# Performance work log

Measured on AMD Instinct MI355X. Metric: run time of the kernel, lower is better.

The kernel has to match this reference:

```python
import jax, jax.numpy as jnp
import numpy as np

T, N, D, G, H = 52, 1000, 2, 150, 50


def _mlp_scalar(x, W1, b1, W2, b2):
    # Elementwise scalar-input MLP: x [T,N,D] -> [T,N,D]
    h = jnp.tanh(x[..., None] * W1[0] + b1)          # [T,N,D,H]
    return jnp.einsum('tndh,h->tnd', h, W2[:, 0]) + b2[0]


def setup_inputs() -> dict:
    key = jax.random.key(0)
    ks = jax.random.split(key, 18)
    f = lambda k, s: jax.random.normal(k, s, dtype=jnp.float32)
    return {
        'TX': f(ks[0], (T, N, D)),
        't': jnp.arange(T, dtype=jnp.float32) * 0.01,
        'gaussn_0': f(ks[1], (G, T - 2, N)),
        'gaussn_1': f(ks[2], (G, T - 2, N, D)),
        'gaussn_2': f(ks[3], (G, T - 2, N, D)),
        'gaussnp1_1': f(ks[4], (G, T - 2, N, D)),
        'gaussnp1_2': f(ks[5], (G, T - 2, N, D)),
        'gaussnp2_0': f(ks[6], (G, T - 2, N)),
        'gaussnp2_1': f(ks[7], (G, T - 2, N, D)),
        'gaussnp2_2': f(ks[8], (G, T - 2, N, D)),
        'Wd1': f(ks[9], (1, H)) * 0.5,
        'bd1': jnp.zeros((H,), jnp.float32),
        'Wd2': f(ks[10], (H, 1)) * (1.0 / np.sqrt(H)),
        'bd2': jnp.zeros((1,), jnp.float32),
        'Ws1': f(ks[11], (1, H)) * 0.5,
        'bs1': jnp.zeros((H,), jnp.float32),
        'Ws2': f(ks[12], (H, 1)) * (1.0 / np.sqrt(H)),
        'bs2': jnp.zeros((1,), jnp.float32),
    }


def reference(TX, t, gaussn_0, gaussn_1, gaussn_2, gaussnp1_1, gaussnp1_2,
              gaussnp2_0, gaussnp2_1, gaussnp2_2,
              Wd1, bd1, Wd2, bd2, Ws1, bs1, Ws2, bs2):
    n = TX.shape[1]
    drift = _mlp_scalar(TX, Wd1, bd1, Wd2, bd2)            # [T,N,D]
    Dh = 0.5 * _mlp_scalar(TX, Ws1, bs1, Ws2, bs2)          # [T,N,D]

    def proj(g1, g2, a):
        # sum over d then mean over n == einsum over (n,d) / n -> [G, T-2]
        return (jnp.einsum('gtnd,tnd->gt', g1, a[0])
                + jnp.einsum('gtnd,tnd->gt', g2, a[1])) / n

    An = proj(gaussn_1, gaussn_2, (drift[:-2], Dh[:-2]))
    Anp1 = proj(gaussnp1_1, gaussnp1_2, (drift[1:-1], Dh[1:-1]))
    Anp2 = proj(gaussnp2_1, gaussnp2_2, (drift[2:], Dh[2:]))

    dt = (jnp.max(t) - jnp.min(t)) / (TX.shape[0] - 1)
    Aq = (An + 4.0 * Anp1 + Anp2) / 3.0 * dt                # LMM_3
    bq = jnp.mean(gaussnp2_0, axis=2) - jnp.mean(gaussn_0, axis=2)
    return (Aq - bq).reshape(-1)                            # [G*(T-2)]
```

## Files before the change

### kernel.cpp

```cpp
#include <hip/hip_runtime.h>
#include <hip/hip_bf16.h>

#define T_   52
#define N_   1000
#define D_   2
#define G_   150
#define H_   50
#define TM2  (T_ - 2)
#define ND   (N_ * D_)
#define TND  (T_ * N_ * D_)

typedef unsigned short ushort8_t __attribute__((ext_vector_type(8)));
typedef float          float8_t  __attribute__((ext_vector_type(8)));

__device__ __forceinline__ float bf2f(unsigned short u) {
    return __uint_as_float(((unsigned)u) << 16);
}
__device__ __forceinline__ unsigned short f2bf(float f) {
    unsigned u = __float_as_uint(f);
    u += 0x7fffu + ((u >> 16) & 1u);
    return (unsigned short)(u >> 16);
}

template<bool F32>
__device__ __forceinline__ float ld1(const void* p, int i) {
    if constexpr (F32) return ((const float*)p)[i];
    else               return bf2f(((const unsigned short*)p)[i]);
}

template<bool F32>
__device__ __forceinline__ float8_t ld8(const void* p, int i) {
    if constexpr (F32) {
        return *(const float8_t*)((const float*)p + i);
    } else {
        ushort8_t v = *(const ushort8_t*)((const unsigned short*)p + i);
        float8_t r;
#pragma unroll
        for (int j = 0; j < 8; ++j) r[j] = bf2f(v[j]);
        return r;
    }
}

template<bool F32>
__device__ __forceinline__ void mlp_body(
    const void* __restrict__ TX,
    const void* __restrict__ Wd1, const void* __restrict__ bd1,
    const void* __restrict__ Wd2, const void* __restrict__ bd2,
    const void* __restrict__ Ws1, const void* __restrict__ bs1,
    const void* __restrict__ Ws2, const void* __restrict__ bs2,
    float* __restrict__ drift, float* __restrict__ Dh)
{
    __shared__ float sW[6][H_];
    const int tid = threadIdx.x;
    if (tid < H_) {
        sW[0][tid] = ld1<F32>(Wd1, tid);
        sW[1][tid] = ld1<F32>(bd1, tid);
        sW[2][tid] = ld1<F32>(Wd2, tid);
        sW[3][tid] = ld1<F32>(Ws1, tid);
        sW[4][tid] = ld1<F32>(bs1, tid);
        sW[5][tid] = ld1<F32>(Ws2, tid);
    }
    __syncthreads();
    const int i = blockIdx.x * 256 + tid;
    if (i >= TND) return;
    const float x = ld1<F32>(TX, i);
    float accd = 0.f, accs = 0.f;
#pragma unroll 10
    for (int h = 0; h < H_; ++h) {
        accd += tanhf(fmaf(x, sW[0][h], sW[1][h])) * sW[2][h];
        accs += tanhf(fmaf(x, sW[3][h], sW[4][h])) * sW[5][h];
    }
    drift[i] = accd + ld1<F32>(bd2, 0);
    Dh[i]    = 0.5f * (accs + ld1<F32>(bs2, 0));
}

__global__ __launch_bounds__(256) void mlp_kernel(
    const void* TX,
    const void* Wd1, const void* bd1, const void* Wd2, const void* bd2,
    const void* Ws1, const void* bs1, const void* Ws2, const void* bs2,
    const void* t, float* drift, float* Dh)
{
    if (((const unsigned*)t)[0] == 0u)
        mlp_body<true>(TX, Wd1, bd1, Wd2, bd2, Ws1, bs1, Ws2, bs2, drift, Dh);
    else
        mlp_body<false>(TX, Wd1, bd1, Wd2, bd2, Ws1, bs1, Ws2, bs2, drift, Dh);
}

template<bool F32>
__device__ __forceinline__ void proj_body(
    const void* __restrict__ gn0,  const void* __restrict__ gn1,
    const void* __restrict__ gn2,  const void* __restrict__ gp11,
    const void* __restrict__ gp12, const void* __restrict__ gp20,
    const void* __restrict__ gp21, const void* __restrict__ gp22,
    const float* __restrict__ drift, const float* __restrict__ Dh,
    const void* __restrict__ t, void* __restrict__ out)
{
    const int gid = blockIdx.x;
    const int tp  = gid % TM2;
    const int tid = threadIdx.x;

    float acc = 0.f, bacc = 0.f;

    if (tid < ND / 8) {
        const int base = gid * ND + tid * 8;
        const float8_t a1 = ld8<F32>(gn1,  base);
        const float8_t a2 = ld8<F32>(gn2,  base);
        const float8_t b1 = ld8<F32>(gp11, base);
        const float8_t b2 = ld8<F32>(gp12, base);
        const float8_t c1 = ld8<F32>(gp21, base);
        const float8_t c2 = ld8<F32>(gp22, base);
        const int cb = tp * ND + tid * 8;
        const float8_t d0 = *(const float8_t*)(drift + cb);
        const float8_t h0 = *(const float8_t*)(Dh    + cb);
        const float8_t d1 = *(const float8_t*)(drift + cb + ND);
        const float8_t h1 = *(const float8_t*)(Dh    + cb + ND);
        const float8_t d2 = *(const float8_t*)(drift + cb + 2 * ND);
        const float8_t h2 = *(const float8_t*)(Dh    + cb + 2 * ND);
#pragma unroll
        for (int j = 0; j < 8; ++j) {
            acc += a1[j] * d0[j] + a2[j] * h0[j]
                 + 4.f * (b1[j] * d1[j] + b2[j] * h1[j])
                 + c1[j] * d2[j] + c2[j] * h2[j];
        }
    }
    if (tid < N_ / 8) {
        const int b0 = gid * N_ + tid * 8;
        const float8_t z0 = ld8<F32>(gn0,  b0);
        const float8_t z2 = ld8<F32>(gp20, b0);
#pragma unroll
        for (int j = 0; j < 8; ++j) bacc += z2[j] - z0[j];
    }

#pragma unroll
    for (int off = 32; off > 0; off >>= 1) {
        acc  += __shfl_down(acc, off);
        bacc += __shfl_down(bacc, off);
    }
    __shared__ float sA[4], sB[4];
    const int wave = tid >> 6, lane = tid & 63;
    if (lane == 0) { sA[wave] = acc; sB[wave] = bacc; }
    __syncthreads();
    if (tid == 0) {
        const float A = sA[0] + sA[1] + sA[2] + sA[3];
        const float B = sB[0] + sB[1] + sB[2] + sB[3];
        const float dt = (ld1<F32>(t, T_ - 1) - ld1<F32>(t, 0)) * (1.0f / (T_ - 1));
        const float val = A * (dt / (3.0f * (float)N_)) - B * (1.0f / (float)N_);
        if constexpr (F32) ((float*)out)[gid] = val;
        else               ((unsigned short*)out)[gid] = f2bf(val);
    }
}

__global__ __launch_bounds__(256) void proj_kernel(
    const void* gn0,  const void* gn1,  const void* gn2,
    const void* gp11, const void* gp12, const void* gp20,
    const void* gp21, const void* gp22,
    const float* drift, const float* Dh,
    const void* t, void* out)
{
    if (((const unsigned*)t)[0] == 0u)
        proj_body<true>(gn0, gn1, gn2, gp11, gp12, gp20, gp21, gp22,
                        drift, Dh, t, out);
    else
        proj_body<false>(gn0, gn1, gn2, gp11, gp12, gp20, gp21, gp22,
                         drift, Dh, t, out);
}

extern "C" void kernel_launch(void* const* d_in, const int* in_sizes, int n_in,
                              void* d_out, int out_size, void* d_ws, size_t ws_size,
                              hipStream_t stream) {
    const void* TX   = d_in[0];
    const void* t    = d_in[1];
    const void* gn0  = d_in[2];
    const void* gn1  = d_in[3];
    const void* gn2  = d_in[4];
    const void* gp11 = d_in[5];
    const void* gp12 = d_in[6];
    const void* gp20 = d_in[7];
    const void* gp21 = d_in[8];
    const void* gp22 = d_in[9];
    const void* Wd1  = d_in[10];
    const void* bd1  = d_in[11];
    const void* Wd2  = d_in[12];
    const void* bd2  = d_in[13];
    const void* Ws1  = d_in[14];
    const void* bs1  = d_in[15];
    const void* Ws2  = d_in[16];
    const void* bs2  = d_in[17];

    float* drift = (float*)d_ws;
    float* Dh    = drift + TND;

    mlp_kernel<<<(TND + 255) / 256, 256, 0, stream>>>(
        TX, Wd1, bd1, Wd2, bd2, Ws1, bs1, Ws2, bs2, t, drift, Dh);

    proj_kernel<<<G_ * TM2, 256, 0, stream>>>(
        gn0, gn1, gn2, gp11, gp12, gp20, gp21, gp22, drift, Dh, t,
        (void*)d_out);
}
```

Measured before the change: 401.0 us.

## Process CHUNK g-values per block to reuse drift/Dh loads in projection

Each projection block now handles six g indices at one time step instead of a single (g,t) pair. The drift/Dh vectors are loaded once per block and reused across the chunk, and the factor of 4 is folded into them. This cuts redundant workspace reads and the block count from 7500 to 1250. The cost is more registers per thread and fewer blocks, which may reduce latency hiding on a kernel bound by streaming the gaussian arrays.

Result: no change. 403.0 us (+0.5%).

```diff
diff --git a/kernel.cpp b/kernel.cpp
--- a/kernel.cpp
+++ b/kernel.cpp
@@ -9,6 +9,7 @@
 #define TM2  (T_ - 2)
 #define ND   (N_ * D_)
 #define TND  (T_ * N_ * D_)
+#define CHUNK 6
 
 typedef unsigned short ushort8_t __attribute__((ext_vector_type(8)));
 typedef float          float8_t  __attribute__((ext_vector_type(8)));
@@ -95,58 +96,81 @@
     const float* __restrict__ drift, const float* __restrict__ Dh,
     const void* __restrict__ t, void* __restrict__ out)
 {
-    const int gid = blockIdx.x;
-    const int tp  = gid % TM2;
+    const int tp  = blockIdx.x;
+    const int g0  = blockIdx.y * CHUNK;
     const int tid = threadIdx.x;
 
-    float acc = 0.f, bacc = 0.f;
+    float acc[CHUNK], bacc[CHUNK];
+#pragma unroll
+    for (int k = 0; k < CHUNK; ++k) { acc[k] = 0.f; bacc[k] = 0.f; }
 
     if (tid < ND / 8) {
-        const int base = gid * ND + tid * 8;
-        const float8_t a1 = ld8<F32>(gn1,  base);
-        const float8_t a2 = ld8<F32>(gn2,  base);
-        const float8_t b1 = ld8<F32>(gp11, base);
-        const float8_t b2 = ld8<F32>(gp12, base);
-        const float8_t c1 = ld8<F32>(gp21, base);
-        const float8_t c2 = ld8<F32>(gp22, base);
         const int cb = tp * ND + tid * 8;
         const float8_t d0 = *(const float8_t*)(drift + cb);
         const float8_t h0 = *(const float8_t*)(Dh    + cb);
-        const float8_t d1 = *(const float8_t*)(drift + cb + ND);
-        const float8_t h1 = *(const float8_t*)(Dh    + cb + ND);
+        float8_t d1 = *(const float8_t*)(drift + cb + ND);
+        float8_t h1 = *(const float8_t*)(Dh    + cb + ND);
         const float8_t d2 = *(const float8_t*)(drift + cb + 2 * ND);
         const float8_t h2 = *(const float8_t*)(Dh    + cb + 2 * ND);
 #pragma unroll
-        for (int j = 0; j < 8; ++j) {
-            acc += a1[j] * d0[j] + a2[j] * h0[j]
-                 + 4.f * (b1[j] * d1[j] + b2[j] * h1[j])
-                 + c1[j] * d2[j] + c2[j] * h2[j];
+        for (int j = 0; j < 8; ++j) { d1[j] *= 4.f; h1[j] *= 4.f; }
+
+#pragma unroll
+        for (int k = 0; k < CHUNK; ++k) {
+            const int base = ((g0 + k) * TM2 + tp) * ND + tid * 8;
+            const float8_t a1 = ld8<F32>(gn1,  base);
+            const float8_t a2 = ld8<F32>(gn2,  base);
+            const float8_t b1 = ld8<F32>(gp11, base);
+            const float8_t b2 = ld8<F32>(gp12, base);
+            const float8_t c1 = ld8<F32>(gp21, base);
+            const float8_t c2 = ld8<F32>(gp22, base);
+            float s = 0.f;
+#pragma unroll
+            for (int j = 0; j < 8; ++j) {
+                s += a1[j] * d0[j] + a2[j] * h0[j]
+                   + b1[j] * d1[j] + b2[j] * h1[j]
+                   + c1[j] * d2[j] + c2[j] * h2[j];
+            }
+            acc[k] = s;
         }
     }
     if (tid < N_ / 8) {
-        const int b0 = gid * N_ + tid * 8;
-        const float8_t z0 = ld8<F32>(gn0,  b0);
-        const float8_t z2 = ld8<F32>(gp20, b0);
-#pragma unroll
-        for (int j = 0; j < 8; ++j) bacc += z2[j] - z0[j];
+#pragma unroll
+        for (int k = 0; k < CHUNK; ++k) {
+            const int b0 = ((g0 + k) * TM2 + tp) * N_ + tid * 8;
+            const float8_t z0 = ld8<F32>(gn0,  b0);
+            const float8_t z2 = ld8<F32>(gp20, b0);
+            float s = 0.f;
+#pragma unroll
+            for (int j = 0; j < 8; ++j) s += z2[j] - z0[j];
+            bacc[k] = s;
+        }
     }
 
 #pragma unroll
     for (int off = 32; off > 0; off >>= 1) {
-        acc  += __shfl_down(acc, off);
-        bacc += __shfl_down(bacc, off);
-    }
-    __shared__ float sA[4], sB[4];
+#pragma unroll
+        for (int k = 0; k < CHUNK; ++k) {
+            acc[k]  += __shfl_down(acc[k],  off);
+            bacc[k] += __shfl_down(bacc[k], off);
+        }
+    }
+    __shared__ float sA[4][CHUNK], sB[4][CHUNK];
     const int wave = tid >> 6, lane = tid & 63;
-    if (lane == 0) { sA[wave] = acc; sB[wave] = bacc; }
+    if (lane == 0) {
+#pragma unroll
+        for (int k = 0; k < CHUNK; ++k) { sA[wave][k] = acc[k]; sB[wave][k] = bacc[k]; }
+    }
     __syncthreads();
-    if (tid == 0) {
-        const float A = sA[0] + sA[1] + sA[2] + sA[3];
-        const float B = sB[0] + sB[1] + sB[2] + sB[3];
+    if (tid < CHUNK) {
+        float A = 0.f, B = 0.f;
+#pragma unroll
+        for (int w = 0; w < 4; ++w) { A += sA[w][tid]; B += sB[w][tid]; }
         const float dt = (ld1<F32>(t, T_ - 1) - ld1<F32>(t, 0)) * (1.0f / (T_ - 1));
         const float val = A * (dt / (3.0f * (float)N_)) - B * (1.0f / (float)N_);
-        if constexpr (F32) ((float*)out)[gid] = val;
-        else               ((unsigned short*)out)[gid] = f2bf(val);
+        const int oi = (g0 + tid) * TM2 + tp;
+        if constexpr (F32) ((float*)out)[oi] = val;
+        else               ((unsigned short*)out)[oi] = f2bf(val);
     }
 }
 
@@ -193,7 +217,8 @@
     mlp_kernel<<<(TND + 255) / 256, 256, 0, stream>>>(
         TX, Wd1, bd1, Wd2, bd2, Ws1, bs1, Ws2, bs2, t, drift, Dh);
 
-    proj_kernel<<<G_ * TM2, 256, 0, stream>>>(
+    dim3 grid(TM2, G_ / CHUNK);
+    proj_kernel<<<grid, 256, 0, stream>>>(
         gn0, gn1, gn2, gp11, gp12, gp20, gp21, gp22, drift, Dh, t,
         (void*)d_out);
 }
```
